# Kernel tuning notes

Hardware: AMD Instinct MI355X
Metric: run time of the kernel (lower is better)

The kernel has to match this reference:

```python
import jax, jax.numpy as jnp
import numpy as np

N_NODES = 100000
N_EDGES = 1200000
N_PAIRS = 500000
IN_DIM = 128
HID = 64
MLP_HID = 64


def setup_inputs() -> dict:
    key = jax.random.key(0)
    ks = jax.random.split(key, 12)
    x = jax.random.normal(ks[0], (N_NODES, IN_DIM), dtype=jnp.float32)
    graph_edge_index = jax.random.randint(ks[1], (2, N_EDGES), 0, N_NODES, dtype=jnp.int64)
    edge_pairs = jax.random.randint(ks[2], (2, N_PAIRS), 0, N_NODES, dtype=jnp.int64)
    s1 = 1.0 / np.sqrt(IN_DIM)
    s2 = 1.0 / np.sqrt(HID)
    s3 = 1.0 / np.sqrt(4 * HID)
    W1 = jax.random.uniform(ks[3], (IN_DIM, HID), jnp.float32, -s1, s1)
    b1 = jax.random.uniform(ks[4], (HID,), jnp.float32, -s1, s1)
    W2 = jax.random.uniform(ks[5], (HID, HID), jnp.float32, -s2, s2)
    b2 = jax.random.uniform(ks[6], (HID,), jnp.float32, -s2, s2)
    M1 = jax.random.uniform(ks[7], (4 * HID, MLP_HID), jnp.float32, -s3, s3)
    mb1 = jax.random.uniform(ks[8], (MLP_HID,), jnp.float32, -s3, s3)
    M2 = jax.random.uniform(ks[9], (MLP_HID, 1), jnp.float32, -s2, s2)
    mb2 = jax.random.uniform(ks[10], (1,), jnp.float32, -s2, s2)
    return {"x": x, "graph_edge_index": graph_edge_index, "edge_pairs": edge_pairs,
            "W1": W1, "b1": b1, "W2": W2, "b2": b2,
            "M1": M1, "mb1": mb1, "M2": M2, "mb2": mb2}


def gcn_conv(x, W, b, src, dst, n_nodes):
    # PyG GCNConv: h = x @ W; out_i = sum_{(j,i) in E} norm_ji * h_j + self-loop term + b
    # deg includes the added self-loop; norm_ji = deg_j^-1/2 * deg_i^-1/2
    h = x @ W  # [N, H]
    deg = jax.ops.segment_sum(jnp.ones((src.shape[0],), h.dtype), dst,
                              num_segments=n_nodes) + 1.0  # [N]
    dinv = jax.lax.rsqrt(deg)
    coef = dinv[src] * dinv[dst]  # [E]
    agg = jax.ops.segment_sum(h[src] * coef[:, None], dst, num_segments=n_nodes)
    out = agg + h * (1.0 / deg)[:, None] + b  # self-loop norm = deg_i^-1
    return out


def reference(x, graph_edge_index, edge_pairs, W1, b1, W2, b2, M1, mb1, M2, mb2):
    n = x.shape[0]
    src, dst = graph_edge_index[0], graph_edge_index[1]
    # node encoder (dropout = identity in eval mode)
    h = jax.nn.relu(gcn_conv(x, W1, b1, src, dst, n))
    h = jax.nn.relu(gcn_conv(h, W2, b2, src, dst, n))
    # edge head: gather endpoint embeddings, concat [u, v, |u-v|, u*v]
    u = h[edge_pairs[0]]  # [P, H]
    v = h[edge_pairs[1]]  # [P, H]
    feat = jnp.concatenate([u, v, jnp.abs(u - v), u * v], axis=-1)  # [P, 4H]
    z = jax.nn.relu(feat @ M1 + mb1)
    return (z @ M2 + mb2).reshape(-1)  # [P]
```

## Files before the change

kernel.cpp:

```cpp
#include <hip/hip_runtime.h>
#include <math.h>


__global__ void k_count_int(const int* __restrict__ dst, int* __restrict__ cnt, int e) {
  int i = blockIdx.x * blockDim.x + threadIdx.x;
  if (i < e) atomicAdd(&cnt[dst[i]], 1);
}

__global__ void k_dinv(const int* __restrict__ cnt, float* __restrict__ dinv, int n) {
  int i = blockIdx.x * blockDim.x + threadIdx.x;
  if (i < n) dinv[i] = rsqrtf((float)cnt[i] + 1.0f);
}

__global__ __launch_bounds__(256) void k_scan_block(const int* __restrict__ cnt,
                                                    int* __restrict__ rp,
                                                    int* __restrict__ bsum, int n) {
  __shared__ int wsum[4];
  int tid = threadIdx.x;
  int lane = tid & 63, w = tid >> 6;
  int idx = blockIdx.x * 1024 + tid * 4;
  int v0 = (idx + 0 < n) ? cnt[idx + 0] : 0;
  int v1 = (idx + 1 < n) ? cnt[idx + 1] : 0;
  int v2 = (idx + 2 < n) ? cnt[idx + 2] : 0;
  int v3 = (idx + 3 < n) ? cnt[idx + 3] : 0;
  int tot = v0 + v1 + v2 + v3;
  int x = tot;
#pragma unroll
  for (int off = 1; off < 64; off <<= 1) {
    int y = __shfl_up(x, off, 64);
    if (lane >= off) x += y;
  }
  if (lane == 63) wsum[w] = x;
  __syncthreads();
  int woff = 0;
  for (int i = 0; i < w; ++i) woff += wsum[i];
  int run = woff + x - tot;
  if (idx + 0 < n) rp[idx + 0] = run; run += v0;
  if (idx + 1 < n) rp[idx + 1] = run; run += v1;
  if (idx + 2 < n) rp[idx + 2] = run; run += v2;
  if (idx + 3 < n) rp[idx + 3] = run;
  if (tid == 255) bsum[blockIdx.x] = wsum[0] + wsum[1] + wsum[2] + wsum[3];
}

__global__ void k_scan_bsum(int* __restrict__ bsum, int nb) {
  int l = threadIdx.x;
  int v0 = (l < nb) ? bsum[l] : 0;
  int v1 = (64 + l < nb) ? bsum[64 + l] : 0;
  int i0 = v0;
#pragma unroll
  for (int off = 1; off < 64; off <<= 1) {
    int y = __shfl_up(i0, off, 64);
    if (l >= off) i0 += y;
  }
  int T0 = __shfl(i0, 63, 64);
  int i1 = v1;
#pragma unroll
  for (int off = 1; off < 64; off <<= 1) {
    int y = __shfl_up(i1, off, 64);
    if (l >= off) i1 += y;
  }
  if (l < nb) bsum[l] = i0 - v0;
  if (64 + l < nb) bsum[64 + l] = T0 + i1 - v1;
}

__global__ void k_scan_add(int* __restrict__ rp, int* __restrict__ cur,
                           const int* __restrict__ bsum, int n, int e) {
  int i = blockIdx.x * blockDim.x + threadIdx.x;
  if (i < n) {
    int v = rp[i] + bsum[i >> 10];
    rp[i] = v;
    cur[i] = v;
  }
  if (i == 0) rp[n] = e;
}

__global__ void k_fill(const int* __restrict__ src, const int* __restrict__ dst,
                       int* __restrict__ cur, const float* __restrict__ dinv,
                       int* __restrict__ srcs, float* __restrict__ coefs, int e) {
  int i = blockIdx.x * blockDim.x + threadIdx.x;
  if (i >= e) return;
  int s = src[i], d = dst[i];
  int pos = atomicAdd(&cur[d], 1);
  srcs[pos] = s;
  coefs[pos] = dinv[s] * dinv[d];
}

template <int K>
__global__ __launch_bounds__(256) void k_matmul_w(const float* __restrict__ IN,
                                                  const float* __restrict__ W,
                                                  float* __restrict__ OUT,
                                                  int n, int npw) {
  __shared__ float rows[4][K];
  const int wv = threadIdx.x >> 6, lane = threadIdx.x & 63;
  float wreg[K];
#pragma unroll
  for (int k = 0; k < K; ++k) wreg[k] = W[k * 64 + lane];
  int base = (blockIdx.x * 4 + wv) * npw;
  if (base >= n) return;
  int nEnd = base + npw;
  if (nEnd > n) nEnd = n;
  float p0 = IN[(size_t)base * K + lane];
  float p1 = (K == 128) ? IN[(size_t)base * K + 64 + lane] : 0.f;
  for (int node = base; node < nEnd; ++node) {
    rows[wv][lane] = p0;
    if (K == 128) rows[wv][64 + lane] = p1;
    if (node + 1 < nEnd) {
      p0 = IN[(size_t)(node + 1) * K + lane];
      if (K == 128) p1 = IN[(size_t)(node + 1) * K + 64 + lane];
    }
    float a0 = 0.f, a1 = 0.f, a2 = 0.f, a3 = 0.f;
#pragma unroll
    for (int k = 0; k < K; k += 4) {
      float4 xk = *(const float4*)&rows[wv][k];
      a0 = fmaf(xk.x, wreg[k + 0], a0);
      a1 = fmaf(xk.y, wreg[k + 1], a1);
      a2 = fmaf(xk.z, wreg[k + 2], a2);
      a3 = fmaf(xk.w, wreg[k + 3], a3);
    }
    OUT[(size_t)node * 64 + lane] = (a0 + a1) + (a2 + a3);
  }
}

__global__ void k_gather(const float* __restrict__ hlin, const int* __restrict__ rp,
                         const int* __restrict__ srcs, const float* __restrict__ coefs,
                         const float* __restrict__ dinv,
                         const float* __restrict__ bias, float* __restrict__ outB,
                         int n) {
  int warp = threadIdx.x >> 6, lane = threadIdx.x & 63;
  int node = blockIdx.x * 4 + warp;
  if (node >= n) return;
  int g = lane >> 4, l16 = lane & 15;
  int beg = rp[node], end = rp[node + 1];
  int deg = end - beg;
  float dn = dinv[node];
  float ax = 0.f, ay = 0.f, az = 0.f, aw = 0.f;
  for (int base = 0; base < deg; base += 64) {
    int rem = deg - base;
    int m = rem < 64 ? rem : 64;
    int idx = 0;
    float cf = 0.f;
    if (lane < m) {
      idx = srcs[beg + base + lane];
      cf = coefs[beg + base + lane];
    }
    int iters = (m + 3) >> 2;
    for (int i = 0; i < iters; ++i) {
      int k = g + 4 * i;
      int s = __shfl(idx, k, 64);
      float c = __shfl(cf, k, 64);
      float4 h = *(const float4*)(hlin + (size_t)s * 64 + l16 * 4);
      ax = fmaf(h.x, c, ax);
      ay = fmaf(h.y, c, ay);
      az = fmaf(h.z, c, az);
      aw = fmaf(h.w, c, aw);
    }
  }
#pragma unroll
  for (int off = 16; off < 64; off <<= 1) {
    ax += __shfl_xor(ax, off, 64);
    ay += __shfl_xor(ay, off, 64);
    az += __shfl_xor(az, off, 64);
    aw += __shfl_xor(aw, off, 64);
  }
  if (g == 0) {
    float4 hs = *(const float4*)(hlin + (size_t)node * 64 + l16 * 4);
    float4 bb = *(const float4*)(bias + l16 * 4);
    float dd = dn * dn;
    float4 o;
    o.x = ax + hs.x * dd + bb.x;
    o.y = ay + hs.y * dd + bb.y;
    o.z = az + hs.z * dd + bb.z;
    o.w = aw + hs.w * dd + bb.w;
    o.x = o.x > 0.f ? o.x : 0.f;
    o.y = o.y > 0.f ? o.y : 0.f;
    o.z = o.z > 0.f ? o.z : 0.f;
    o.w = o.w > 0.f ? o.w : 0.f;
    *(float4*)(outB + (size_t)node * 64 + l16 * 4) = o;
  }
}

__global__ __launch_bounds__(512, 6) void k_edge_head(
    const float* __restrict__ H, const int* __restrict__ ep,
    const float* __restrict__ M1, const float* __restrict__ mb1,
    const float* __restrict__ M2, const float* __restrict__ mb2,
    float* __restrict__ out, int p_total) {
  __shared__ float sbuf[8192];

  const int tid = threadIdx.x;
  const int pair0 = blockIdx.x * 256;

  const int pi = tid & 255;
  const int hf = tid >> 8;
  const int gp_pi = pair0 + pi;
  const bool valid = gp_pi < p_total;
  int node = 0;
  if (valid) node = hf ? ep[p_total + gp_pi] : ep[gp_pi];
  float* __restrict__ myb = sbuf + hf * 4096;

  const int lane = tid & 63;
  const int w = tid >> 6;
  const int cg = __builtin_amdgcn_readfirstlane(w);
  const int p0 = 4 * lane;

  float acc[8][4];
#pragma unroll
  for (int c = 0; c < 8; ++c)
#pragma unroll
    for (int p = 0; p < 4; ++p) acc[c][p] = 0.f;

  float4 st0, st1, st2, st3;

#pragma unroll
  for (int ph = 0; ph < 4; ++ph) {
    if (ph) __syncthreads();
    if (valid) {
      float4 c0, c1, c2, c3;
      if ((ph & 1) == 0) {
        const float4* hr = (const float4*)(H + (size_t)node * 64 + ph * 16);
        c0 = hr[0]; c1 = hr[1]; c2 = hr[2]; c3 = hr[3];
        st0 = hr[4]; st1 = hr[5]; st2 = hr[6]; st3 = hr[7];
      } else {
        c0 = st0; c1 = st1; c2 = st2; c3 = st3;
      }
      myb[0 * 256 + pi]  = c0.x; myb[1 * 256 + pi]  = c0.y;
      myb[2 * 256 + pi]  = c0.z; myb[3 * 256 + pi]  = c0.w;
      myb[4 * 256 + pi]  = c1.x; myb[5 * 256 + pi]  = c1.y;
      myb[6 * 256 + pi]  = c1.z; myb[7 * 256 + pi]  = c1.w;
      myb[8 * 256 + pi]  = c2.x; myb[9 * 256 + pi]  = c2.y;
      myb[10 * 256 + pi] = c2.z; myb[11 * 256 + pi] = c2.w;
      myb[12 * 256 + pi] = c3.x; myb[13 * 256 + pi] = c3.y;
      myb[14 * 256 + pi] = c3.z; myb[15 * 256 + pi] = c3.w;
    } else {
#pragma unroll
      for (int j = 0; j < 16; ++j) myb[j * 256 + pi] = 0.f;
    }
    __syncthreads();

#pragma unroll 2
    for (int t = 0; t < 16; ++t) {
      float4 u4 = *(const float4*)&sbuf[t * 256 + p0];
      float4 v4 = *(const float4*)&sbuf[4096 + t * 256 + p0];
      float uu[4] = {u4.x, u4.y, u4.z, u4.w};
      float vv[4] = {v4.x, v4.y, v4.z, v4.w};
      float dd[4], mm[4];
#pragma unroll
      for (int p = 0; p < 4; ++p) {
        dd[p] = fabsf(uu[p] - vv[p]);
        mm[p] = uu[p] * vv[p];
      }
      const int tt = ph * 16 + t;
      const float* r0 = M1 + (size_t)tt * 64 + cg * 8;
      const float* r1 = r0 + 64 * 64;
      const float* r2 = r0 + 128 * 64;
      const float* r3 = r0 + 192 * 64;
#pragma unroll
      for (int c = 0; c < 8; ++c) {
        float w0 = r0[c], w1 = r1[c], w2 = r2[c], w3 = r3[c];
#pragma unroll
        for (int p = 0; p < 4; ++p) {
          acc[c][p] = fmaf(uu[p], w0, acc[c][p]);
          acc[c][p] = fmaf(vv[p], w1, acc[c][p]);
          acc[c][p] = fmaf(dd[p], w2, acc[c][p]);
          acc[c][p] = fmaf(mm[p], w3, acc[c][p]);
        }
      }
    }
  }

  __syncthreads();

#pragma unroll
  for (int p = 0; p < 4; ++p) {
    float part = 0.f;
#pragma unroll
    for (int c = 0; c < 8; ++c) {
      float z = acc[c][p] + mb1[cg * 8 + c];
      z = z > 0.f ? z : 0.f;
      part = fmaf(z, M2[cg * 8 + c], part);
    }
    sbuf[w * 256 + p0 + p] = part;
  }
  __syncthreads();

  if (tid < 256) {
    int gp = pair0 + tid;
    if (gp < p_total) {
      float s = 0.f;
#pragma unroll
      for (int w8 = 0; w8 < 8; ++w8) s += sbuf[w8 * 256 + tid];
      out[gp] = s + mb2[0];
    }
  }
}

extern "C" void kernel_launch(void* const* d_in, const int* in_sizes, int n_in,
                              void* d_out, int out_size, void* d_ws, size_t ws_size,
                              hipStream_t stream) {
  const float* x   = (const float*)d_in[0];
  const int*   gei = (const int*)d_in[1];
  const int*   ep  = (const int*)d_in[2];
  const float* W1  = (const float*)d_in[3];
  const float* b1  = (const float*)d_in[4];
  const float* W2  = (const float*)d_in[5];
  const float* b2  = (const float*)d_in[6];
  const float* M1  = (const float*)d_in[7];
  const float* mb1 = (const float*)d_in[8];
  const float* M2  = (const float*)d_in[9];
  const float* mb2 = (const float*)d_in[10];
  float* out = (float*)d_out;

  const int N = in_sizes[0] / 128;
  const int E = in_sizes[1] / 2;
  const int P = in_sizes[2] / 2;
  const int* src = gei;
  const int* dst = gei + E;

  char* ws = (char*)d_ws;
  auto align256 = [](size_t b) { return (b + 255) & ~(size_t)255; };
  size_t degBytes  = align256((size_t)N * 4);
  size_t hBytes    = align256((size_t)N * 64 * 4);
  size_t cntBytes  = align256((size_t)N * 4);
  size_t rpBytes   = align256((size_t)(N + 1) * 4);
  size_t srcBytes  = align256((size_t)E * 4);

  size_t off = 0;
  float* dinv  = (float*)(ws + off); off += degBytes;
  float* A     = (float*)(ws + off); off += hBytes;
  float* B     = (float*)(ws + off); off += hBytes;
  int*   cnt   = (int*)(ws + off);   off += cntBytes;
  int*   rp    = (int*)(ws + off);   off += rpBytes;
  int*   srcs  = (int*)(ws + off);   off += srcBytes;
  float* coefs = (float*)(ws + off); off += srcBytes;
  int*   bsum  = (int*)(ws + off);

  const int BLK = 256;
  const int nb = (N + 1023) / 1024;

  hipMemsetAsync(cnt, 0, (size_t)N * 4, stream);
  k_count_int<<<(E + BLK - 1) / BLK, BLK, 0, stream>>>(dst, cnt, E);
  k_dinv<<<(N + BLK - 1) / BLK, BLK, 0, stream>>>(cnt, dinv, N);
  k_scan_block<<<nb, BLK, 0, stream>>>(cnt, rp, bsum, N);
  k_scan_bsum<<<1, 64, 0, stream>>>(bsum, nb);
  k_scan_add<<<(N + BLK - 1) / BLK, BLK, 0, stream>>>(rp, cnt, bsum, N, E);
  k_fill<<<(E + BLK - 1) / BLK, BLK, 0, stream>>>(src, dst, cnt, dinv, srcs, coefs, E);

  const int NPW = 16;
  const int mmGrid = (N + 4 * NPW - 1) / (4 * NPW);

  k_matmul_w<128><<<mmGrid, BLK, 0, stream>>>(x, W1, A, N, NPW);
  k_gather<<<(N + 3) / 4, BLK, 0, stream>>>(A, rp, srcs, coefs, dinv, b1, B, N);

  k_matmul_w<64><<<mmGrid, BLK, 0, stream>>>(B, W2, A, N, NPW);
  k_gather<<<(N + 3) / 4, BLK, 0, stream>>>(A, rp, srcs, coefs, dinv, b2, B, N);

  k_edge_head<<<(P + 255) / 256, 512, 0, stream>>>(B, ep, M1, mb1, M2, mb2, out, P);
}
```

Measured before the change: 483.4 us.

## Fold GCN normalization into matmul output and drop per-edge coefficients

Scales each node's linear output by dinv[src] inside the matmul, so the gather only sums neighbour rows and applies dinv[dst] once per node. This removes the per-edge coefficient array, its writes in k_fill and its reads and shuffles in the gather, and merges the dinv computation into the scan-add kernel. The gather is also unrolled four-way, with padding lanes pointing at a zeroed dummy row N so the unrolled loop stays branch-free. The cost is one extra memset and a per-node multiply in the matmul, plus extra loads of the zero row for padded iterations.

```diff
diff --git a/kernel.cpp b/kernel.cpp
--- a/kernel.cpp
+++ b/kernel.cpp
@@ -5,11 +5,6 @@
 __global__ void k_count_int(const int* __restrict__ dst, int* __restrict__ cnt, int e) {
   int i = blockIdx.x * blockDim.x + threadIdx.x;
   if (i < e) atomicAdd(&cnt[dst[i]], 1);
-}
-
-__global__ void k_dinv(const int* __restrict__ cnt, float* __restrict__ dinv, int n) {
-  int i = blockIdx.x * blockDim.x + threadIdx.x;
-  if (i < n) dinv[i] = rsqrtf((float)cnt[i] + 1.0f);
 }
 
 __global__ __launch_bounds__(256) void k_scan_block(const int* __restrict__ cnt,
@@ -64,30 +59,31 @@
 }
 
 __global__ void k_scan_add(int* __restrict__ rp, int* __restrict__ cur,
-                           const int* __restrict__ bsum, int n, int e) {
+                           float* __restrict__ dinv, const int* __restrict__ bsum,
+                           int n, int e) {
   int i = blockIdx.x * blockDim.x + threadIdx.x;
   if (i < n) {
+    int c = cur[i];
     int v = rp[i] + bsum[i >> 10];
     rp[i] = v;
     cur[i] = v;
+    dinv[i] = rsqrtf((float)c + 1.0f);
   }
   if (i == 0) rp[n] = e;
 }
 
 __global__ void k_fill(const int* __restrict__ src, const int* __restrict__ dst,
-                       int* __restrict__ cur, const float* __restrict__ dinv,
-                       int* __restrict__ srcs, float* __restrict__ coefs, int e) {
+                       int* __restrict__ cur, int* __restrict__ srcs, int e) {
   int i = blockIdx.x * blockDim.x + threadIdx.x;
   if (i >= e) return;
-  int s = src[i], d = dst[i];
-  int pos = atomicAdd(&cur[d], 1);
-  srcs[pos] = s;
-  coefs[pos] = dinv[s] * dinv[d];
+  int pos = atomicAdd(&cur[dst[i]], 1);
+  srcs[pos] = src[i];
 }
 
 template <int K>
 __global__ __launch_bounds__(256) void k_matmul_w(const float* __restrict__ IN,
                                                   const float* __restrict__ W,
+                                                  const float* __restrict__ dscale,
                                                   float* __restrict__ OUT,
                                                   int n, int npw) {
   __shared__ float rows[4][K];
@@ -117,13 +113,12 @@
       a2 = fmaf(xk.z, wreg[k + 2], a2);
       a3 = fmaf(xk.w, wreg[k + 3], a3);
     }
-    OUT[(size_t)node * 64 + lane] = (a0 + a1) + (a2 + a3);
+    OUT[(size_t)node * 64 + lane] = ((a0 + a1) + (a2 + a3)) * dscale[node];
   }
 }
 
 __global__ void k_gather(const float* __restrict__ hlin, const int* __restrict__ rp,
-                         const int* __restrict__ srcs, const float* __restrict__ coefs,
-                         const float* __restrict__ dinv,
+                         const int* __restrict__ srcs, const float* __restrict__ dinv,
                          const float* __restrict__ bias, float* __restrict__ outB,
                          int n) {
   int warp = threadIdx.x >> 6, lane = threadIdx.x & 63;
@@ -137,22 +132,24 @@
   for (int base = 0; base < deg; base += 64) {
     int rem = deg - base;
     int m = rem < 64 ? rem : 64;
-    int idx = 0;
-    float cf = 0.f;
-    if (lane < m) {
-      idx = srcs[beg + base + lane];
-      cf = coefs[beg + base + lane];
-    }
+    int idx = n;
+    if (lane < m) idx = srcs[beg + base + lane];
     int iters = (m + 3) >> 2;
-    for (int i = 0; i < iters; ++i) {
-      int k = g + 4 * i;
-      int s = __shfl(idx, k, 64);
-      float c = __shfl(cf, k, 64);
-      float4 h = *(const float4*)(hlin + (size_t)s * 64 + l16 * 4);
-      ax = fmaf(h.x, c, ax);
-      ay = fmaf(h.y, c, ay);
-      az = fmaf(h.z, c, az);
-      aw = fmaf(h.w, c, aw);
+    int itr4 = (iters + 3) & ~3;
+    for (int i = 0; i < itr4; i += 4) {
+      int k0 = g + 4 * i;
+      int s0 = __shfl(idx, k0, 64);
+      int s1 = __shfl(idx, k0 + 4, 64);
+      int s2 = __shfl(idx, k0 + 8, 64);
+      int s3 = __shfl(idx, k0 + 12, 64);
+      float4 h0 = *(const float4*)(hlin + (size_t)s0 * 64 + l16 * 4);
+      float4 h1 = *(const float4*)(hlin + (size_t)s1 * 64 + l16 * 4);
+      float4 h2 = *(const float4*)(hlin + (size_t)s2 * 64 + l16 * 4);
+      float4 h3 = *(const float4*)(hlin + (size_t)s3 * 64 + l16 * 4);
+      ax += h0.x; ay += h0.y; az += h0.z; aw += h0.w;
+      ax += h1.x; ay += h1.y; az += h1.z; aw += h1.w;
+      ax += h2.x; ay += h2.y; az += h2.z; aw += h2.w;
+      ax += h3.x; ay += h3.y; az += h3.z; aw += h3.w;
     }
   }
 #pragma unroll
@@ -165,12 +162,11 @@
   if (g == 0) {
     float4 hs = *(const float4*)(hlin + (size_t)node * 64 + l16 * 4);
     float4 bb = *(const float4*)(bias + l16 * 4);
-    float dd = dn * dn;
     float4 o;
-    o.x = ax + hs.x * dd + bb.x;
-    o.y = ay + hs.y * dd + bb.y;
-    o.z = az + hs.z * dd + bb.z;
-    o.w = aw + hs.w * dd + bb.w;
+    o.x = dn * (ax + hs.x) + bb.x;
+    o.y = dn * (ay + hs.y) + bb.y;
+    o.z = dn * (az + hs.z) + bb.z;
+    o.w = dn * (aw + hs.w) + bb.w;
     o.x = o.x > 0.f ? o.x : 0.f;
     o.y = o.y > 0.f ? o.y : 0.f;
     o.z = o.z > 0.f ? o.z : 0.f;
@@ -318,7 +314,7 @@
   char* ws = (char*)d_ws;
   auto align256 = [](size_t b) { return (b + 255) & ~(size_t)255; };
   size_t degBytes  = align256((size_t)N * 4);
-  size_t hBytes    = align256((size_t)N * 64 * 4);
+  size_t hBytes    = align256((size_t)(N + 1) * 64 * 4);
   size_t cntBytes  = align256((size_t)N * 4);
   size_t rpBytes   = align256((size_t)(N + 1) * 4);
   size_t srcBytes  = align256((size_t)E * 4);
@@ -330,28 +326,27 @@
   int*   cnt   = (int*)(ws + off);   off += cntBytes;
   int*   rp    = (int*)(ws + off);   off += rpBytes;
   int*   srcs  = (int*)(ws + off);   off += srcBytes;
-  float* coefs = (float*)(ws + off); off += srcBytes;
   int*   bsum  = (int*)(ws + off);
 
   const int BLK = 256;
   const int nb = (N + 1023) / 1024;
 
   hipMemsetAsync(cnt, 0, (size_t)N * 4, stream);
+  hipMemsetAsync(A + (size_t)N * 64, 0, 64 * 4, stream);
   k_count_int<<<(E + BLK - 1) / BLK, BLK, 0, stream>>>(dst, cnt, E);
-  k_dinv<<<(N + BLK - 1) / BLK, BLK, 0, stream>>>(cnt, dinv, N);
   k_scan_block<<<nb, BLK, 0, stream>>>(cnt, rp, bsum, N);
   k_scan_bsum<<<1, 64, 0, stream>>>(bsum, nb);
-  k_scan_add<<<(N + BLK - 1) / BLK, BLK, 0, stream>>>(rp, cnt, bsum, N, E);
-  k_fill<<<(E + BLK - 1) / BLK, BLK, 0, stream>>>(src, dst, cnt, dinv, srcs, coefs, E);
+  k_scan_add<<<(N + BLK - 1) / BLK, BLK, 0, stream>>>(rp, cnt, dinv, bsum, N, E);
+  k_fill<<<(E + BLK - 1) / BLK, BLK, 0, stream>>>(src, dst, cnt, srcs, E);
 
   const int NPW = 16;
   const int mmGrid = (N + 4 * NPW - 1) / (4 * NPW);
 
-  k_matmul_w<128><<<mmGrid, BLK, 0, stream>>>(x, W1, A, N, NPW);
-  k_gather<<<(N + 3) / 4, BLK, 0, stream>>>(A, rp, srcs, coefs, dinv, b1, B, N);
-
-  k_matmul_w<64><<<mmGrid, BLK, 0, stream>>>(B, W2, A, N, NPW);
-  k_gather<<<(N + 3) / 4, BLK, 0, stream>>>(A, rp, srcs, coefs, dinv, b2, B, N);
+  k_matmul_w<128><<<mmGrid, BLK, 0, stream>>>(x, W1, dinv, A, N, NPW);
+  k_gather<<<(N + 3) / 4, BLK, 0, stream>>>(A, rp, srcs, dinv, b1, B, N);
+
+  k_matmul_w<64><<<mmGrid, BLK, 0, stream>>>(B, W2, dinv, A, N, NPW);
+  k_gather<<<(N + 3) / 4, BLK, 0, stream>>>(A, rp, srcs, dinv, b2, B, N);
 
   k_edge_head<<<(P + 255) / 256, 512, 0, stream>>>(B, ep, M1, mb1, M2, mb2, out, P);
 }
```

Measured after the change: 490.8 us. Within noise of the previous version (+1.5%).
